# Optimization experiments

Measured on AMD Instinct MI355X. Metric: run time of the kernel, lower is better.

Reference implementation:

```python
import jax, jax.numpy as jnp
import numpy as np

SCALE = 64.0
MARGIN = 0.5
N = 16_777_216  # number of samples


def setup_inputs() -> dict:
    key = jax.random.key(0)
    k1, k2 = jax.random.split(key)
    dist = jax.random.normal(k1, (2, N), dtype=jnp.float32)
    label = jax.random.randint(k2, (N,), 0, 2, dtype=jnp.int32)
    return {"dist": dist, "label": label}


def reference(dist, label):
    # Vectorized form of the per-sample loop:
    #   loss_i = -log( exp(s*cos(d[y_i,i]+m)) / (exp(s*cos(d[y_i,i]+m)) + exp(s*cos(d[1-y_i,i]))) )
    idx = jnp.arange(dist.shape[1])
    pos = dist[label, idx]        # d[label_i, i]
    neg = dist[1 - label, idx]    # d[1-label_i, i]
    lp = SCALE * jnp.cos(pos + MARGIN)
    ln = SCALE * jnp.cos(neg)
    # -log(exp(lp)/(exp(lp)+exp(ln))) = logaddexp(lp, ln) - lp  (numerically stable)
    loss = jnp.sum(jnp.logaddexp(lp, ln) - lp)
    return loss
```

## Files before the change

### kernel.cpp

```cpp
#include <hip/hip_runtime.h>

#define SCALE 64.0f
#define MARGIN 0.5f

constexpr int BLOCK = 256;
constexpr int GRID = 2048;

__device__ __forceinline__ float cos_fast(float x) {
    float r = x * 0.15915494309189535f;
    r = r - floorf(r);
    return __builtin_amdgcn_cosf(r);
}

__device__ __forceinline__ float sample_loss(float d0, float d1, int lab) {
    float pos = lab ? d1 : d0;
    float neg = lab ? d0 : d1;
    float c1 = cos_fast(pos + MARGIN);
    float c0 = cos_fast(neg);
    float d  = (c0 - c1) * SCALE;
    float t  = __expf(-fabsf(d));
    float s  = __logf(1.0f + t);
    return fmaxf(d, 0.0f) + s;
}

__device__ __forceinline__ float block_reduce(float acc) {
    #pragma unroll
    for (int off = 32; off > 0; off >>= 1)
        acc += __shfl_down(acc, off, 64);
    __shared__ float warp_sums[BLOCK / 64];
    int wave = threadIdx.x >> 6;
    int lane = threadIdx.x & 63;
    if (lane == 0) warp_sums[wave] = acc;
    __syncthreads();
    if (threadIdx.x == 0) {
        float s = warp_sums[0];
        #pragma unroll
        for (int w = 1; w < BLOCK / 64; ++w) s += warp_sums[w];
        return s;
    }
    return 0.0f;
}

__global__ __launch_bounds__(BLOCK) void loss_partial_kernel(
    const float* __restrict__ dist, const int* __restrict__ label,
    float* __restrict__ partial, int n)
{
    const int nvec = n >> 2;
    const float4* __restrict__ row0 = reinterpret_cast<const float4*>(dist);
    const float4* __restrict__ row1 = reinterpret_cast<const float4*>(dist + n);
    const int4*   __restrict__ lab4 = reinterpret_cast<const int4*>(label);

    float acc = 0.0f;
    for (int i = blockIdx.x * BLOCK + threadIdx.x; i < nvec; i += gridDim.x * BLOCK) {
        float4 a = row0[i];
        float4 b = row1[i];
        int4   l = lab4[i];
        acc += sample_loss(a.x, b.x, l.x);
        acc += sample_loss(a.y, b.y, l.y);
        acc += sample_loss(a.z, b.z, l.z);
        acc += sample_loss(a.w, b.w, l.w);
    }

    float s = block_reduce(acc);
    if (threadIdx.x == 0) partial[blockIdx.x] = s;
}

__global__ __launch_bounds__(BLOCK) void reduce_partials_kernel(
    const float* __restrict__ partial, float* __restrict__ out, int nparts)
{
    float acc = 0.0f;
    for (int i = threadIdx.x; i < nparts; i += BLOCK) acc += partial[i];
    float s = block_reduce(acc);
    if (threadIdx.x == 0) out[0] = s;
}

extern "C" void kernel_launch(void* const* d_in, const int* in_sizes, int n_in,
                              void* d_out, int out_size, void* d_ws, size_t ws_size,
                              hipStream_t stream) {
    const float* dist  = (const float*)d_in[0];
    const int*   label = (const int*)d_in[1];
    float* out = (float*)d_out;
    float* partial = (float*)d_ws;

    const int n = in_sizes[0] / 2;

    loss_partial_kernel<<<GRID, BLOCK, 0, stream>>>(dist, label, partial, n);
    reduce_partials_kernel<<<1, BLOCK, 0, stream>>>(partial, out, GRID);
}
```

Baseline: 40.03 us.

## Replace grid-stride loop with one-shot blocks processing two vec4 groups per thread

Removes the fixed 2048-block grid-stride loop and launches enough blocks so each thread processes exactly two float4 groups, issuing all six vector loads before computing. This aims to increase memory-level parallelism and remove loop overhead in a bandwidth-bound kernel. In exchange it launches many more blocks, each doing a block reduction and partial write, and the final single-block reduction sums four times as many partials.

```diff
diff --git a/kernel.cpp b/kernel.cpp
--- a/kernel.cpp
+++ b/kernel.cpp
@@ -4,7 +4,7 @@
 #define MARGIN 0.5f
 
 constexpr int BLOCK = 256;
-constexpr int GRID = 2048;
+constexpr int GPT = 2;
 
 __device__ __forceinline__ float cos_fast(float x) {
     float r = x * 0.15915494309189535f;
@@ -21,6 +21,15 @@
     float t  = __expf(-fabsf(d));
     float s  = __logf(1.0f + t);
     return fmaxf(d, 0.0f) + s;
+}
+
+__device__ __forceinline__ float quad_loss(float4 a, float4 b, int4 l) {
+    float acc;
+    acc  = sample_loss(a.x, b.x, l.x);
+    acc += sample_loss(a.y, b.y, l.y);
+    acc += sample_loss(a.z, b.z, l.z);
+    acc += sample_loss(a.w, b.w, l.w);
+    return acc;
 }
 
 __device__ __forceinline__ float block_reduce(float acc) {
@@ -45,20 +54,26 @@
     const float* __restrict__ dist, const int* __restrict__ label,
     float* __restrict__ partial, int n)
 {
-    const int nvec = n >> 2;
+    const int ngroups = n >> 2;
     const float4* __restrict__ row0 = reinterpret_cast<const float4*>(dist);
     const float4* __restrict__ row1 = reinterpret_cast<const float4*>(dist + n);
     const int4*   __restrict__ lab4 = reinterpret_cast<const int4*>(label);
 
+    const int g0 = blockIdx.x * (BLOCK * GPT) + threadIdx.x;
+    const int g1 = g0 + BLOCK;
+
     float acc = 0.0f;
-    for (int i = blockIdx.x * BLOCK + threadIdx.x; i < nvec; i += gridDim.x * BLOCK) {
-        float4 a = row0[i];
-        float4 b = row1[i];
-        int4   l = lab4[i];
-        acc += sample_loss(a.x, b.x, l.x);
-        acc += sample_loss(a.y, b.y, l.y);
-        acc += sample_loss(a.z, b.z, l.z);
-        acc += sample_loss(a.w, b.w, l.w);
+    if (g1 < ngroups) {
+        float4 a0 = row0[g0];
+        float4 a1 = row0[g1];
+        float4 b0 = row1[g0];
+        float4 b1 = row1[g1];
+        int4   l0 = lab4[g0];
+        int4   l1 = lab4[g1];
+        acc  = quad_loss(a0, b0, l0);
+        acc += quad_loss(a1, b1, l1);
+    } else if (g0 < ngroups) {
+        acc = quad_loss(row0[g0], row1[g0], lab4[g0]);
     }
 
     float s = block_reduce(acc);
@@ -83,7 +98,9 @@
     float* partial = (float*)d_ws;
 
     const int n = in_sizes[0] / 2;
+    const int ngroups = n >> 2;
+    const int grid = (ngroups + BLOCK * GPT - 1) / (BLOCK * GPT);
 
-    loss_partial_kernel<<<GRID, BLOCK, 0, stream>>>(dist, label, partial, n);
-    reduce_partials_kernel<<<1, BLOCK, 0, stream>>>(partial, out, GRID);
+    loss_partial_kernel<<<grid, BLOCK, 0, stream>>>(dist, label, partial, n);
+    reduce_partials_kernel<<<1, BLOCK, 0, stream>>>(partial, out, grid);
 }
```

Result: slower. 43.59 us (+8.9%).
